# Kernel tuning notes

Hardware: AMD Instinct MI355X
Metric: run time of the kernel (lower is better)

The kernel has to match this reference:

```python
import jax, jax.numpy as jnp
import numpy as np

NUM_GROUPS = 32
EPS = 1e-5


def group_norm(x, scale, bias):
    # x: [B, C, H, W]
    B, C, H, W = x.shape
    g = x.reshape(B, NUM_GROUPS, C // NUM_GROUPS * H * W)
    mean = g.mean(axis=-1, keepdims=True)
    var = g.var(axis=-1, keepdims=True)
    g = (g - mean) * jax.lax.rsqrt(var + EPS)
    g = g.reshape(B, C, H, W)
    return g * scale[None, :, None, None] + bias[None, :, None, None]


def conv1x1(x, w, b):
    # x: [B, C, H, W], w: [O, C], b: [O]
    return jnp.einsum('bchw,oc->bohw', x, w) + b[None, :, None, None]


def setup_inputs() -> dict:
    key = jax.random.key(0)
    ks = jax.random.split(key, 11)
    B, C, H, W = 32, 256, 32, 32
    s = 1.0 / np.sqrt(C)
    return {
        'x': jax.random.normal(ks[0], (B, C, H, W), jnp.float32),
        'gn_scale': jnp.ones((C,), jnp.float32),
        'gn_bias': jnp.zeros((C,), jnp.float32),
        'wq': jax.random.normal(ks[1], (C, C), jnp.float32) * s,
        'bq': jnp.zeros((C,), jnp.float32),
        'wk': jax.random.normal(ks[2], (C, C), jnp.float32) * s,
        'bk': jnp.zeros((C,), jnp.float32),
        'wv': jax.random.normal(ks[3], (C, C), jnp.float32) * s,
        'bv': jnp.zeros((C,), jnp.float32),
        'wo': jax.random.normal(ks[4], (C, C), jnp.float32) * s,
        'bo': jnp.zeros((C,), jnp.float32),
    }


def reference(x, gn_scale, gn_bias, wq, bq, wk, bk, wv, bv, wo, bo):
    B, C, H, W = x.shape
    h = group_norm(x, gn_scale, gn_bias)
    q = conv1x1(h, wq, bq).reshape(B, C, H * W)  # [B, C, N]
    k = conv1x1(h, wk, bk).reshape(B, C, H * W)
    v = conv1x1(h, wv, bv).reshape(B, C, H * W)
    # scores: [B, N, N]
    w = jnp.einsum('bcn,bcm->bnm', q, k) * (C ** -0.5)
    w = jax.nn.softmax(w, axis=-1)
    o = jnp.einsum('bnm,bcm->bcn', w, v).reshape(B, C, H, W)
    o = conv1x1(o, wo, bo)
    return x + o
```

## Files before the change

kernel.cpp:

```cpp
#include <hip/hip_runtime.h>

typedef __attribute__((ext_vector_type(4))) float f32x4;
typedef __attribute__((ext_vector_type(16))) float f32x16;
typedef __attribute__((ext_vector_type(8))) short bf16x8;

__device__ __forceinline__ unsigned short f2bf(float f) {
  union { float f; unsigned u; } v; v.f = f;
  unsigned r = (v.u + 0x7FFFu + ((v.u >> 16) & 1u)) >> 16;
  return (unsigned short)r;
}

__device__ __forceinline__ unsigned cvt_pk_bf16(float lo, float hi) {
  unsigned r;
  asm("v_cvt_pk_bf16_f32 %0, %1, %2" : "=v"(r) : "v"(lo), "v"(hi));
  return r;
}

__device__ __forceinline__ void load16_lds(const void* g, void* l) {
  __builtin_amdgcn_global_load_lds(
      (__attribute__((address_space(1))) void*)(uintptr_t)g,
      (__attribute__((address_space(3))) void*)(unsigned int)(uintptr_t)l,
      16, 0, 0);
}

#define QSCALE 0.09016844f

__global__ __launch_bounds__(256) void gn_conv_kernel(
    const float* __restrict__ x, const float* __restrict__ gamma,
    const float* __restrict__ beta, unsigned short* __restrict__ h,
    const float* __restrict__ wq, const float* __restrict__ wk,
    const float* __restrict__ wv, const float* __restrict__ wo,
    const float* __restrict__ bq, const float* __restrict__ bk,
    unsigned short* __restrict__ wqkb, unsigned short* __restrict__ wvb,
    unsigned short* __restrict__ wob, float* __restrict__ bqkf) {
  __shared__ float xs[8 * 1024];
  __shared__ float red[16];
  const int t = threadIdx.x;

  if (blockIdx.x >= 1024) {
    const int wblk = blockIdx.x - 1024;
    const float* src[4] = {wq, wk, wv, wo};
    unsigned short* dst[4] = {wqkb, wqkb + 65536, wvb, wob};
    const int ti = wblk >> 2, part = wblk & 3;
    const float sc = (ti == 0) ? QSCALE : 1.f;
    const float* s = src[ti];
    unsigned short* d = dst[ti];
#pragma unroll
    for (int j = 0; j < 16; ++j) {
      int idx = part * 4096 + j * 256 + t;
      float4 v = ((const float4*)s)[idx];
      ushort4 r;
      r.x = f2bf(v.x * sc); r.y = f2bf(v.y * sc);
      r.z = f2bf(v.z * sc); r.w = f2bf(v.w * sc);
      ((ushort4*)d)[idx] = r;
    }
    if (wblk == 0) {
      bqkf[t] = bq[t] * QSCALE;
      bqkf[256 + t] = bk[t];
    }
    return;
  }

  const int b = blockIdx.x >> 5, g = blockIdx.x & 31;
  const float* xp = x + (size_t)(b * 256 + g * 8) * 1024;
  float s = 0.f, ss = 0.f;
#pragma unroll
  for (int j = 0; j < 8; ++j) {
    float4 v = ((const float4*)xp)[j * 256 + t];
    ((float4*)xs)[j * 256 + t] = v;
    s += v.x + v.y + v.z + v.w;
    ss += v.x * v.x + v.y * v.y + v.z * v.z + v.w * v.w;
  }
#pragma unroll
  for (int o = 32; o >= 1; o >>= 1) {
    s += __shfl_xor(s, o);
    ss += __shfl_xor(ss, o);
  }
  const int wave = t >> 6, lane = t & 63;
  if (lane == 0) { red[wave] = s; red[wave + 4] = ss; }
  __syncthreads();
  s = red[0] + red[1] + red[2] + red[3];
  ss = red[4] + red[5] + red[6] + red[7];
  float mean = s * (1.f / 8192.f);
  float var = ss * (1.f / 8192.f) - mean * mean;
  float rstd = rsqrtf(var + 1e-5f);
  float a[8], c[8];
#pragma unroll
  for (int ci = 0; ci < 8; ++ci) {
    float gm = gamma[g * 8 + ci], bt = beta[g * 8 + ci];
    a[ci] = rstd * gm;
    c[ci] = bt - mean * rstd * gm;
  }
  unsigned short* hb = h + (size_t)b * 1024 * 256 + g * 8;
#pragma unroll
  for (int j = 0; j < 4; ++j) {
    int n = j * 256 + t;
    float f0 = xs[0 * 1024 + n] * a[0] + c[0];
    float f1 = xs[1 * 1024 + n] * a[1] + c[1];
    float f2 = xs[2 * 1024 + n] * a[2] + c[2];
    float f3 = xs[3 * 1024 + n] * a[3] + c[3];
    float f4 = xs[4 * 1024 + n] * a[4] + c[4];
    float f5 = xs[5 * 1024 + n] * a[5] + c[5];
    float f6 = xs[6 * 1024 + n] * a[6] + c[6];
    float f7 = xs[7 * 1024 + n] * a[7] + c[7];
    uint4 o4;
    o4.x = (unsigned)f2bf(f0) | ((unsigned)f2bf(f1) << 16);
    o4.y = (unsigned)f2bf(f2) | ((unsigned)f2bf(f3) << 16);
    o4.z = (unsigned)f2bf(f4) | ((unsigned)f2bf(f5) << 16);
    o4.w = (unsigned)f2bf(f6) | ((unsigned)f2bf(f7) << 16);
    *(uint4*)(hb + (size_t)n * 256) = o4;
  }
}

template <bool OUT_F32, bool HAS_RES>
__device__ __forceinline__ void gemm_core(
    const unsigned short* __restrict__ Ab, const unsigned short* __restrict__ Bb,
    void* __restrict__ Cb, const float* __restrict__ bias, int bias_mode,
    const float* __restrict__ res, int bm, int bn, int N, int K,
    unsigned short* As, unsigned short* Bs) {
  const int t = threadIdx.x;
  const int wave = t >> 6, lane = t & 63;
  const int wm = (wave >> 1) * 64, wn = (wave & 1) * 64;
  const int srow = t >> 2, schunk = t & 3;
  const int lrow = lane & 15, kg = lane >> 4;

  f32x4 acc[4][4] = {};

#pragma unroll
  for (int r = 0; r < 2; ++r) {
    int row = r * 64 + srow;
    int cs = schunk ^ ((row >> 1) & 3);
    load16_lds(Ab + (size_t)(bm + row) * K + cs * 8, &As[(r * 64 + wave * 16) * 32]);
    load16_lds(Bb + (size_t)(bn + row) * K + cs * 8, &Bs[(r * 64 + wave * 16) * 32]);
  }
  asm volatile("s_waitcnt vmcnt(0)" ::: "memory");
  __builtin_amdgcn_s_barrier();
  __builtin_amdgcn_sched_barrier(0);

  const int nk = K >> 5;
  for (int kt = 0; kt < nk; ++kt) {
    const int cur = kt & 1;
    if (kt + 1 < nk) {
      const int k0 = (kt + 1) << 5;
      const int boff = (cur ^ 1) * 4096;
#pragma unroll
      for (int r = 0; r < 2; ++r) {
        int row = r * 64 + srow;
        int cs = schunk ^ ((row >> 1) & 3);
        load16_lds(Ab + (size_t)(bm + row) * K + (k0 + cs * 8), &As[boff + (r * 64 + wave * 16) * 32]);
        load16_lds(Bb + (size_t)(bn + row) * K + (k0 + cs * 8), &Bs[boff + (r * 64 + wave * 16) * 32]);
      }
    }
    const int boff = cur * 4096;
    bf16x8 af[4], bfr[4];
#pragma unroll
    for (int i = 0; i < 4; ++i) {
      int ra = wm + i * 16 + lrow;
      af[i] = *(const bf16x8*)&As[boff + ra * 32 + ((kg ^ ((ra >> 1) & 3)) * 8)];
      int rb = wn + i * 16 + lrow;
      bfr[i] = *(const bf16x8*)&Bs[boff + rb * 32 + ((kg ^ ((rb >> 1) & 3)) * 8)];
    }
    __builtin_amdgcn_s_setprio(1);
#pragma unroll
    for (int i = 0; i < 4; ++i)
#pragma unroll
      for (int j = 0; j < 4; ++j)
        acc[i][j] = __builtin_amdgcn_mfma_f32_16x16x32_bf16(af[i], bfr[j], acc[i][j], 0, 0, 0);
    __builtin_amdgcn_s_setprio(0);
    asm volatile("s_waitcnt vmcnt(0) lgkmcnt(0)" ::: "memory");
    __builtin_amdgcn_s_barrier();
    __builtin_amdgcn_sched_barrier(0);
  }

#pragma unroll
  for (int i = 0; i < 4; ++i) {
#pragma unroll
    for (int j = 0; j < 4; ++j) {
#pragma unroll
      for (int r = 0; r < 4; ++r) {
        int m = bm + wm + i * 16 + kg * 4 + r;
        int n = bn + wn + j * 16 + lrow;
        float v = acc[i][j][r];
        v += (bias_mode == 1) ? bias[m] : bias[n];
        if constexpr (HAS_RES) v += res[(size_t)m * N + n];
        if constexpr (OUT_F32)
          ((float*)Cb)[(size_t)m * N + n] = v;
        else
          ((unsigned short*)Cb)[(size_t)m * N + n] = f2bf(v);
      }
    }
  }
}

__global__ __launch_bounds__(256) void proj_kernel(
    const unsigned short* __restrict__ h, const unsigned short* __restrict__ wqkb,
    const unsigned short* __restrict__ wvb, unsigned short* __restrict__ qkb,
    unsigned short* __restrict__ vtb, const float* __restrict__ bqkf,
    const float* __restrict__ bv) {
  __shared__ unsigned short As[2 * 4096];
  __shared__ unsigned short Bs[2 * 4096];
  const int tid = blockIdx.x;
  const int bz = blockIdx.y;
  const long long sHN = 1024LL * 256, sQK = 1024LL * 512;
  if (tid < 32) {
    int bn = (tid & 3) * 128, bm = (tid >> 2) * 128;
    gemm_core<false, false>(h + bz * sHN, wqkb, qkb + bz * sQK,
                            bqkf, 2, nullptr, bm, bn, 512, 256, As, Bs);
  } else {
    int t2 = tid - 32;
    int bn = (t2 & 7) * 128, bm = (t2 >> 3) * 128;
    gemm_core<false, false>(wvb, h + bz * sHN, vtb + bz * sHN,
                            bv, 1, nullptr, bm, bn, 1024, 256, As, Bs);
  }
}

__global__ __launch_bounds__(256) void out_kernel(
    const unsigned short* __restrict__ wob, const unsigned short* __restrict__ ot,
    float* __restrict__ out, const float* __restrict__ bo,
    const float* __restrict__ x) {
  __shared__ unsigned short As[2 * 4096];
  __shared__ unsigned short Bs[2 * 4096];
  const int tid = blockIdx.x;
  const int bz = blockIdx.y;
  const long long sHN = 1024LL * 256;
  int bn = (tid & 7) * 128, bm = (tid >> 3) * 128;
  gemm_core<true, true>(wob, ot + bz * sHN, out + bz * sHN,
                        bo, 1, x + bz * sHN, bm, bn, 1024, 256, As, Bs);
}

__global__ __launch_bounds__(512, 2) void flash_attn(
    const unsigned short* __restrict__ qk,
    const unsigned short* __restrict__ vt,
    unsigned short* __restrict__ ot) {
  __shared__ unsigned short SMEM[81920];
  const int VS = 32768, PB = 65536;

  const int t = threadIdx.x;
  const int wave = t >> 6, lane = t & 63;
  const int wr = wave >> 1, wh = wave & 1;
  const int lrow = lane & 15, hi = lane >> 4;
  const int l31 = lane & 31, h2 = lane >> 5;

  const int lbid = blockIdx.x;
  const int logical = (lbid & 7) * 32 + (lbid >> 3);
  const int b = logical >> 3;
  const int q0 = (logical & 7) * 128;

  const unsigned short* qb = qk + (size_t)b * 1024 * 512;
  const unsigned short* kb = qb + 256;
  const unsigned short* vb = vt + (size_t)b * 1024 * 256;

#pragma unroll
  for (int p = 0; p < 4; ++p) {
    int row = p * 16 + wave * 2 + (lane >> 5);
    int ch = l31 ^ (row & 31);
    load16_lds(kb + (size_t)row * 512 + ch * 8, &SMEM[(p * 16 + wave * 2) * 256]);
  }

  bf16x8 aq[16];
#pragma unroll
  for (int kk = 0; kk < 16; ++kk)
    aq[kk] = *(const bf16x8*)(qb + (size_t)(q0 + wr * 32 + l31) * 512 + kk * 16 + h2 * 8);

  f32x4 acco[2][8] = {};
  float lsum = 0.f;

  asm volatile("s_waitcnt vmcnt(0)" ::: "memory");
  __builtin_amdgcn_s_barrier();
  __builtin_amdgcn_sched_barrier(0);

  for (int tt = 0; tt <= 16; ++tt) {
    const int cur = tt & 1, nxt = cur ^ 1;

    if (tt < 15) {
      const unsigned short* kn = kb + (size_t)(tt + 1) * 64 * 512;
#pragma unroll
      for (int p = 0; p < 4; ++p) {
        int row = p * 16 + wave * 2 + (lane >> 5);
        int ch = l31 ^ (row & 31);
        load16_lds(kn + (size_t)row * 512 + ch * 8, &SMEM[nxt * 16384 + (p * 16 + wave * 2) * 256]);
      }
    }
    if (tt < 16) {
      const unsigned short* vn = vb + tt * 64;
#pragma unroll
      for (int p = 0; p < 4; ++p) {
        int row = p * 64 + wave * 8 + (lane >> 3);
        int ch = (lane & 7) ^ (row & 7);
        load16_lds(vn + (size_t)row * 1024 + ch * 8, &SMEM[VS + cur * 16384 + (p * 64 + wave * 8) * 64]);
      }
    }

    f32x16 accs = {};
    if (tt < 16) {
      const int kbase = cur * 16384;
      const int krow = (wh * 32 + l31) * 256;
      __builtin_amdgcn_s_setprio(1);
#pragma unroll
      for (int kk = 0; kk < 16; ++kk) {
        bf16x8 kf = *(const bf16x8*)&SMEM[kbase + krow + (((kk * 2 + h2) ^ l31) << 3)];
        accs = __builtin_amdgcn_mfma_f32_32x32x16_bf16(kf, aq[kk], accs, 0, 0, 0);
      }
      __builtin_amdgcn_s_setprio(0);
    }

    if (tt >= 1) {
      const unsigned short* Pp = &SMEM[PB + nxt * 8192];
      const unsigned short* Vp = &SMEM[VS + nxt * 16384];
      const int qa0 = wr * 32 + lrow;
      const int qa1 = qa0 + 16;
      const int rot0 = (lrow >> 3) & 3;
      const int rot1 = (rot0 + 2) & 3;
#pragma unroll
      for (int kk2 = 0; kk2 < 2; ++kk2) {
        bf16x8 pa0 = *(const bf16x8*)&Pp[qa0 * 64 + ((((kk2 * 4 + hi + 2 * rot0) & 7) ^ (qa0 & 7)) << 3)];
        bf16x8 pa1 = *(const bf16x8*)&Pp[qa1 * 64 + ((((kk2 * 4 + hi + 2 * rot1) & 7) ^ (qa1 & 7)) << 3)];
        __builtin_amdgcn_s_setprio(1);
#pragma unroll
        for (int jj = 0; jj < 8; ++jj) {
          int c = wh * 128 + jj * 16 + lrow;
          bf16x8 bv8 = *(const bf16x8*)&Vp[c * 64 + (((kk2 * 4 + hi) ^ (c & 7)) * 8)];
          acco[0][jj] = __builtin_amdgcn_mfma_f32_16x16x32_bf16(pa0, bv8, acco[0][jj], 0, 0, 0);
          acco[1][jj] = __builtin_amdgcn_mfma_f32_16x16x32_bf16(pa1, bv8, acco[1][jj], 0, 0, 0);
        }
        __builtin_amdgcn_s_setprio(0);
      }
    }

    if (tt < 16) {
      char* Pw = (char*)&SMEM[PB + cur * 8192];
      const int q = wr * 32 + l31;
      const int qx = q & 7;
      const int rot2 = (l31 >> 3) & 3;
      const int qoff = q * 128 + (h2 << 3);
#pragma unroll
      for (int m = 0; m < 4; ++m) {
        float e0 = __builtin_amdgcn_exp2f(accs[4 * m + 0]);
        float e1 = __builtin_amdgcn_exp2f(accs[4 * m + 1]);
        float e2 = __builtin_amdgcn_exp2f(accs[4 * m + 2]);
        float e3 = __builtin_amdgcn_exp2f(accs[4 * m + 3]);
        lsum += (e0 + e1) + (e2 + e3);
        uint2 w2;
        w2.x = cvt_pk_bf16(e0, e1);
        w2.y = cvt_pk_bf16(e2, e3);
        int physc = ((wh * 4 + m + 2 * rot2) & 7) ^ qx;
        *(uint2*)(Pw + qoff + (physc << 4)) = w2;
      }
    }

    asm volatile("s_waitcnt vmcnt(0) lgkmcnt(0)" ::: "memory");
    __builtin_amdgcn_s_barrier();
    __builtin_amdgcn_sched_barrier(0);
  }

  lsum += __shfl_xor(lsum, 32);
  float* lred = (float*)SMEM;
  if (lane < 32) lred[wave * 32 + lane] = lsum;
  __syncthreads();

  unsigned short* ob = ot + (size_t)b * 1024 * 256;
#pragma unroll
  for (int i = 0; i < 2; ++i) {
    float inv[4];
#pragma unroll
    for (int r = 0; r < 4; ++r) {
      int rl = wr * 32 + i * 16 + hi * 4 + r;
      inv[r] = 1.f / (lred[wr * 64 + (rl & 31)] + lred[wr * 64 + 32 + (rl & 31)]);
    }
#pragma unroll
    for (int jj = 0; jj < 8; ++jj)
#pragma unroll
      for (int r = 0; r < 4; ++r) {
        int n = q0 + wr * 32 + i * 16 + hi * 4 + r;
        int c = wh * 128 + jj * 16 + lrow;
        ob[(size_t)n * 256 + c] = f2bf(acco[i][jj][r] * inv[r]);
      }
  }
}

extern "C" void kernel_launch(void* const* d_in, const int* in_sizes, int n_in,
                              void* d_out, int out_size, void* d_ws, size_t ws_size,
                              hipStream_t stream) {
  const float* x    = (const float*)d_in[0];
  const float* gnsc = (const float*)d_in[1];
  const float* gnb  = (const float*)d_in[2];
  const float* wq   = (const float*)d_in[3];
  const float* bq   = (const float*)d_in[4];
  const float* wk   = (const float*)d_in[5];
  const float* bk   = (const float*)d_in[6];
  const float* wv   = (const float*)d_in[7];
  const float* bv   = (const float*)d_in[8];
  const float* wo   = (const float*)d_in[9];
  const float* bo   = (const float*)d_in[10];
  float* out = (float*)d_out;

  unsigned short* wqkb = (unsigned short*)d_ws;
  unsigned short* wvb  = wqkb + 131072;
  unsigned short* wob  = wvb + 65536;
  float*          bqkf = (float*)(wob + 65536);
  unsigned short* h    = wob + 65536 + 2048;
  unsigned short* qkb  = h + 8388608;
  unsigned short* vt   = qkb + 16777216;
  unsigned short* ot   = h;

  gn_conv_kernel<<<dim3(1040), 256, 0, stream>>>(
      x, gnsc, gnb, h, wq, wk, wv, wo, bq, bk, wqkb, wvb, wob, bqkf);
  proj_kernel<<<dim3(48, 32), 256, 0, stream>>>(h, wqkb, wvb, qkb, vt, bqkf, bv);
  flash_attn<<<dim3(256), 512, 0, stream>>>(qkb, vt, ot);
  out_kernel<<<dim3(16, 32), 256, 0, stream>>>(wob, ot, out, bo, x);
}
```

Measured before the change: 118.2 us.

## Load V fragments directly into registers and single-buffer P in LDS

The flash attention kernel now loads V tiles straight from global memory into registers for the PV MFMA, instead of staging them in a double-buffered LDS region. The P tile becomes single-buffered, with an extra barrier between the PV reads and the next P write. Shared memory drops from 160KB to 80KB, and the P swizzle loses its rotation term. The tradeoffs are more VGPRs, uncached-by-LDS global reads of V that each wave issues redundantly, an extra barrier per iteration, and possibly more bank conflicts on P.

```diff
diff --git a/kernel.cpp b/kernel.cpp
--- a/kernel.cpp
+++ b/kernel.cpp
@@ -232,8 +232,8 @@
     const unsigned short* __restrict__ qk,
     const unsigned short* __restrict__ vt,
     unsigned short* __restrict__ ot) {
-  __shared__ unsigned short SMEM[81920];
-  const int VS = 32768, PB = 65536;
+  __shared__ unsigned short SMEM[40960];
+  const int PB = 32768;
 
   const int t = threadIdx.x;
   const int wave = t >> 6, lane = t & 63;
@@ -252,7 +252,7 @@
 
 #pragma unroll
   for (int p = 0; p < 4; ++p) {
-    int row = p * 16 + wave * 2 + (lane >> 5);
+    int row = p * 16 + wave * 2 + h2;
     int ch = l31 ^ (row & 31);
     load16_lds(kb + (size_t)row * 512 + ch * 8, &SMEM[(p * 16 + wave * 2) * 256]);
   }
@@ -272,22 +272,25 @@
   for (int tt = 0; tt <= 16; ++tt) {
     const int cur = tt & 1, nxt = cur ^ 1;
 
+    bf16x8 vreg[16];
+    if (tt >= 1) {
+      const unsigned short* vn = vb + (tt - 1) * 64;
+#pragma unroll
+      for (int kk2 = 0; kk2 < 2; ++kk2)
+#pragma unroll
+        for (int jj = 0; jj < 8; ++jj) {
+          int c = wh * 128 + jj * 16 + lrow;
+          vreg[kk2 * 8 + jj] = *(const bf16x8*)(vn + (size_t)c * 1024 + kk2 * 32 + hi * 8);
+        }
+    }
+
     if (tt < 15) {
       const unsigned short* kn = kb + (size_t)(tt + 1) * 64 * 512;
 #pragma unroll
       for (int p = 0; p < 4; ++p) {
-        int row = p * 16 + wave * 2 + (lane >> 5);
+        int row = p * 16 + wave * 2 + h2;
         int ch = l31 ^ (row & 31);
         load16_lds(kn + (size_t)row * 512 + ch * 8, &SMEM[nxt * 16384 + (p * 16 + wave * 2) * 256]);
-      }
-    }
-    if (tt < 16) {
-      const unsigned short* vn = vb + tt * 64;
-#pragma unroll
-      for (int p = 0; p < 4; ++p) {
-        int row = p * 64 + wave * 8 + (lane >> 3);
-        int ch = (lane & 7) ^ (row & 7);
-        load16_lds(vn + (size_t)row * 1024 + ch * 8, &SMEM[VS + cur * 16384 + (p * 64 + wave * 8) * 64]);
       }
     }
 
@@ -305,33 +308,31 @@
     }
 
     if (tt >= 1) {
-      const unsigned short* Pp = &SMEM[PB + nxt * 8192];
-      const unsigned short* Vp = &SMEM[VS + nxt * 16384];
+      const unsigned short* Pp = &SMEM[PB];
       const int qa0 = wr * 32 + lrow;
       const int qa1 = qa0 + 16;
-      const int rot0 = (lrow >> 3) & 3;
-      const int rot1 = (rot0 + 2) & 3;
 #pragma unroll
       for (int kk2 = 0; kk2 < 2; ++kk2) {
-        bf16x8 pa0 = *(const bf16x8*)&Pp[qa0 * 64 + ((((kk2 * 4 + hi + 2 * rot0) & 7) ^ (qa0 & 7)) << 3)];
-        bf16x8 pa1 = *(const bf16x8*)&Pp[qa1 * 64 + ((((kk2 * 4 + hi + 2 * rot1) & 7) ^ (qa1 & 7)) << 3)];
+        bf16x8 pa0 = *(const bf16x8*)&Pp[qa0 * 64 + ((kk2 * 32 + hi * 8) ^ ((qa0 & 7) << 3))];
+        bf16x8 pa1 = *(const bf16x8*)&Pp[qa1 * 64 + ((kk2 * 32 + hi * 8) ^ ((qa1 & 7) << 3))];
         __builtin_amdgcn_s_setprio(1);
 #pragma unroll
         for (int jj = 0; jj < 8; ++jj) {
-          int c = wh * 128 + jj * 16 + lrow;
-          bf16x8 bv8 = *(const bf16x8*)&Vp[c * 64 + (((kk2 * 4 + hi) ^ (c & 7)) * 8)];
-          acco[0][jj] = __builtin_amdgcn_mfma_f32_16x16x32_bf16(pa0, bv8, acco[0][jj], 0, 0, 0);
-          acco[1][jj] = __builtin_amdgcn_mfma_f32_16x16x32_bf16(pa1, bv8, acco[1][jj], 0, 0, 0);
+          acco[0][jj] = __builtin_amdgcn_mfma_f32_16x16x32_bf16(pa0, vreg[kk2 * 8 + jj], acco[0][jj], 0, 0, 0);
+          acco[1][jj] = __builtin_amdgcn_mfma_f32_16x16x32_bf16(pa1, vreg[kk2 * 8 + jj], acco[1][jj], 0, 0, 0);
         }
         __builtin_amdgcn_s_setprio(0);
       }
     }
 
+    asm volatile("s_waitcnt lgkmcnt(0)" ::: "memory");
+    __builtin_amdgcn_s_barrier();
+    __builtin_amdgcn_sched_barrier(0);
+
     if (tt < 16) {
-      char* Pw = (char*)&SMEM[PB + cur * 8192];
+      char* Pw = (char*)&SMEM[PB];
       const int q = wr * 32 + l31;
       const int qx = q & 7;
-      const int rot2 = (l31 >> 3) & 3;
       const int qoff = q * 128 + (h2 << 3);
 #pragma unroll
       for (int m = 0; m < 4; ++m) {
@@ -343,7 +344,7 @@
         uint2 w2;
         w2.x = cvt_pk_bf16(e0, e1);
         w2.y = cvt_pk_bf16(e2, e3);
-        int physc = ((wh * 4 + m + 2 * rot2) & 7) ^ qx;
+        int physc = (wh * 4 + m) ^ qx;
         *(uint2*)(Pw + qoff + (physc << 4)) = w2;
       }
     }
```

Result: slower. 190.9 us (+61.4%).
